# Performance work log

Hardware: AMD Instinct MI355X
Metric: run time of the kernel (lower is better)

## Reference

```python
import jax, jax.numpy as jnp
import numpy as np

NUM_COEFF = 32   # num_coeff_per_dim
NUM_POINTS = 64  # Chebyshev collocation points
MAX_ITERS = 10
TOL = 0.01
BATCH, DIM, HID, T_EVAL_N = 512, 256, 512, 16


def T_grid(t, n):
    # Chebyshev T_k(t), k=0..n-1 -> [n, len(t)]
    rows = [jnp.ones_like(t), t]
    for _ in range(2, n):
        rows.append(2.0 * t * rows[-1] - rows[-2])
    return jnp.stack(rows[:n])


def U_grid(t, n):
    rows = [jnp.ones_like(t), 2.0 * t]
    for _ in range(2, n):
        rows.append(2.0 * t * rows[-1] - rows[-2])
    return jnp.stack(rows[:n])


def DT_grid(t, n):
    # d/dt T_k = k * U_{k-1}
    return jnp.vstack([jnp.zeros((1, t.shape[0]), t.dtype),
                       U_grid(t, n - 1) * jnp.arange(1, n, dtype=t.dtype)[:, None]])


def vf_point(t, y, W1, b1, W2, b2):
    # f(t, y) for y [B, D], scalar t
    h = jnp.tanh(y @ W1 + b1 + t)
    return h @ W2 + b2


def vf_grid(t, y, W1, b1, W2, b2):
    # vectorized over Chebyshev points: y [B, D, P], t [P]
    h = jnp.tanh(jnp.einsum('bdp,dh->bhp', y, W1) + b1[None, :, None] + t[None, None, :])
    return jnp.einsum('bhp,hd->bdp', h, W2) + b2[None, :, None]


def setup_inputs() -> dict:
    key = jax.random.key(0)
    ks = jax.random.split(key, 7)
    s1 = 1.0 / np.sqrt(DIM)
    s2 = 1.0 / np.sqrt(HID)
    return {
        'y_init': jax.random.normal(ks[0], (BATCH, DIM), jnp.float32),
        't_eval': jnp.linspace(0.0, 1.0, T_EVAL_N, dtype=jnp.float32),
        'B_init': jax.random.uniform(ks[1], (BATCH, DIM, NUM_COEFF - 2), jnp.float32),
        'W1': jax.random.normal(ks[2], (DIM, HID), jnp.float32) * s1,
        'b1': jax.random.normal(ks[3], (HID,), jnp.float32) * 0.1,
        'W2': jax.random.normal(ks[4], (HID, DIM), jnp.float32) * s2,
        'b2': jax.random.normal(ks[5], (DIM,), jnp.float32) * 0.1,
    }


def _pan_solve(y_init, t_eval, B_init, W1, b1, W2, b2):
    t0, t1 = t_eval[0], t_eval[-1]
    dt = t_eval.dtype
    # time-independent spectral operators
    t_cheb = -jnp.sign(t1 - t0) * jnp.cos(jnp.pi * jnp.arange(NUM_POINTS, dtype=dt) / NUM_POINTS)
    Dt = jnp.diff(jnp.concatenate([t_cheb, jnp.ones((1,), dt)]))
    Phi = T_grid(t_cheb, NUM_COEFF)                        # [N, P]
    DPhi = (2.0 / (t1 - t0)) * DT_grid(t_cheb, NUM_COEFF)  # [N, P]
    inv0 = jnp.linalg.inv(jnp.stack([Phi[0:2, 0], DPhi[0:2, 0]]).T)  # [2,2]
    PD2 = jnp.stack([Phi[2:, 0], DPhi[2:, 0]], axis=-1)    # [N-2, 2]
    D01 = jnp.stack([DPhi[0, :], DPhi[1, :]], axis=0)      # [2, P]
    Phi_b = DPhi[2:, :] - PD2 @ inv0 @ D01                 # [N-2, P]
    Q = jnp.linalg.inv(Phi_b @ (Dt[:, None] * Phi_b.T))    # [N-2, N-2]
    PhibTQ = (Dt[:, None] * Phi_b.T) @ Q                   # [P, N-2]
    M2 = inv0 @ D01 @ PhibTQ                               # [2, N-2]

    f_init = vf_point(t0, y_init, W1, b1, W2, b2)
    yf2 = jnp.stack([y_init, f_init], axis=-1)             # [B, D, 2]

    def head(B_tail):
        return (yf2 - B_tail @ PD2) @ inv0                 # [B, D, 2]

    B = B_init
    done = jnp.array(False)
    delta = jnp.array(jnp.inf, dt)
    iters = jnp.array(0, jnp.int32)
    for _ in range(MAX_ITERS):  # Picard fixed-point iteration (masked early stop)
        B_prev = B
        B_full = jnp.concatenate([head(B_prev), B_prev], axis=-1)  # [B, D, N]
        y_grid = jnp.einsum('bdn,np->bdp', B_full, Phi)            # [B, D, P]
        fapprox = vf_grid(t_cheb, y_grid, W1, b1, W2, b2)          # [B, D, P]
        B_new = jnp.einsum('bdp,pn->bdn', fapprox, PhibTQ) - yf2 @ M2
        d = jnp.linalg.norm(B_new - B_prev)
        B = jnp.where(done, B_prev, B_new)
        delta = jnp.where(done, delta, d)
        iters = jnp.where(done, iters, iters + 1)
        done = done | (d < TOL)

    B_full = jnp.concatenate([head(B), B], axis=-1)
    t_out = -1.0 + 2.0 * (t_eval - t0) / (t1 - t0)
    Phi_out = T_grid(t_out, NUM_COEFF)                     # [N, T]
    traj = jnp.einsum('bdn,nt->tbd', B_full, Phi_out)      # [T, B, D]
    return traj, B, delta, iters


def reference(y_init, t_eval, B_init, W1, b1, W2, b2):
    traj, B, delta, iters = _pan_solve(y_init, t_eval, B_init, W1, b1, W2, b2)
    return (t_eval, traj, delta, B)
```

## Files before the change

### kernel.cpp

```cpp
#include <hip/hip_runtime.h>
#include <math.h>

#define NBATCH 512
#define NDIM 256
#define NHID 512
#define NC 32
#define NTAIL 30
#define NP 64
#define TEV 16
#define MAXIT 10
#define TOLF 0.01f
#define PI_F 3.14159265358979323846f

typedef __bf16 bf16_t;
typedef __bf16 bf16x8 __attribute__((ext_vector_type(8)));
typedef float f32x4 __attribute__((ext_vector_type(4)));
typedef unsigned short ushort_t;

constexpr size_t OFF_TCHEB = 0;
constexpr size_t OFF_PHIT  = 64;
constexpr size_t OFF_PD2I  = 2112;
constexpr size_t OFF_M2    = 2176;
constexpr size_t OFF_INV0  = 2240;
constexpr size_t OFF_PHIOUT= 2256;
constexpr size_t OFF_PQ    = 2768;
constexpr size_t OFF_PQBH  = 4816;
constexpr size_t OFF_PQBL  = 5840;
constexpr size_t OFF_PHIH  = 6864;
constexpr size_t OFF_PHIL  = 7888;
constexpr size_t OFF_SCAL  = 8912;
constexpr size_t OFF_H1F   = 8928;
constexpr size_t OFF_YF2I  = OFF_H1F + 262144;
constexpr size_t OFF_YFR   = OFF_YF2I + 262144;
constexpr size_t OFF_BT    = OFF_YFR + 3932160;
constexpr size_t OFF_W1T   = OFF_BT + 3932160;
constexpr size_t OFF_W2T   = OFF_W1T + 65536;
constexpr size_t WS_FLOATS = OFF_W2T + 65536;

constexpr size_t OUT_TEVAL = 0;
constexpr size_t OUT_TRAJ  = 16;
constexpr size_t OUT_DELTA = 16 + (size_t)TEV*NBATCH*NDIM;
constexpr size_t OUT_B     = OUT_DELTA + 1;

__device__ __forceinline__ ushort_t bf16bits(float v) {
    bf16_t h = (bf16_t)v; ushort_t u; __builtin_memcpy(&u, &h, 2); return u;
}
__device__ __forceinline__ float bf16val(ushort_t u) {
    bf16_t h; __builtin_memcpy(&h, &u, 2); return (float)h;
}

__global__ __launch_bounds__(512) void prologue_kernel(
    const float* __restrict__ t_eval, const float* __restrict__ y,
    const float* __restrict__ Bin,
    const float* __restrict__ W1, const float* __restrict__ b1,
    const float* __restrict__ W2, const float* __restrict__ b2,
    float* __restrict__ ws, float* __restrict__ out)
{
    struct SetupSh {
        double Gaug[30][61];
        double rowk[60];
        double colk[30];
        float Phi[32][64];
        float DPhi[32][64];
        float Phib[30][64];
        float tcs[64];
        float DtS[64];
        float inv0s[4];
        float pd2s[30][2];
    };
    __shared__ __align__(16) char pm[40960];
    static_assert(sizeof(SetupSh) <= 40960, "SetupSh too big");

    const int tid = threadIdx.x;
    const int role = blockIdx.x;

    if (role == 0) {
        SetupSh& S = *(SetupSh*)pm;
        const float t0 = t_eval[0], t1 = t_eval[TEV-1];
        const float sgn = (t1 > t0) ? 1.f : -1.f;

        if (tid < 64) {
            const float t = -sgn * cosf(PI_F * (float)tid / 64.f);
            S.tcs[tid] = t;
            float p0 = 1.f, p1 = t;
            S.Phi[0][tid] = p0; S.Phi[1][tid] = p1;
            for (int k = 2; k < 32; ++k) { float pk = 2.f*t*p1 - p0; S.Phi[k][tid] = pk; p0 = p1; p1 = pk; }
            const float sc = 2.f / (t1 - t0);
            float u0 = 1.f, u1 = 2.f*t;
            S.DPhi[0][tid] = 0.f;
            S.DPhi[1][tid] = sc * 1.f * u0;
            S.DPhi[2][tid] = sc * 2.f * u1;
            for (int k = 3; k < 32; ++k) { float uk = 2.f*t*u1 - u0; S.DPhi[k][tid] = sc * (float)k * uk; u0 = u1; u1 = uk; }
        }
        __syncthreads();
        if (tid < 64) S.DtS[tid] = ((tid < 63) ? S.tcs[tid+1] : 1.0f) - S.tcs[tid];
        if (tid == 0) {
            double a = S.Phi[0][0], b = S.DPhi[0][0], c = S.Phi[1][0], d = S.DPhi[1][0];
            double det = a*d - b*c;
            S.inv0s[0] = (float)( d/det); S.inv0s[1] = (float)(-b/det);
            S.inv0s[2] = (float)(-c/det); S.inv0s[3] = (float)( a/det);
        }
        __syncthreads();
        if (tid < 30) {
            float P = S.Phi[2+tid][0], D = S.DPhi[2+tid][0];
            float a0 = P*S.inv0s[0] + D*S.inv0s[2];
            float a1 = P*S.inv0s[1] + D*S.inv0s[3];
            S.pd2s[tid][0] = a0; S.pd2s[tid][1] = a1;
            ws[OFF_PD2I + tid*2+0] = a0;
            ws[OFF_PD2I + tid*2+1] = a1;
        }
        __syncthreads();
        if (tid < 64)
            for (int m = 0; m < 30; ++m)
                S.Phib[m][tid] = S.DPhi[2+m][tid] - (S.pd2s[m][0]*S.DPhi[0][tid] + S.pd2s[m][1]*S.DPhi[1][tid]);
        __syncthreads();

        for (int e = tid; e < 900; e += 512) {
            int i = e / 30, j = e % 30;
            double s = 0.0;
            for (int p = 0; p < 64; ++p) s += (double)S.Phib[i][p] * (double)S.DtS[p] * (double)S.Phib[j][p];
            S.Gaug[i][j] = s;
            S.Gaug[i][30+j] = (i == j) ? 1.0 : 0.0;
        }
        __syncthreads();

        for (int k = 0; k < 30; ++k) {
            double invpv = 1.0 / S.Gaug[k][k];
            if (tid < 60) S.rowk[tid] = S.Gaug[k][tid] * invpv;
            if (tid >= 64 && tid < 94) S.colk[tid-64] = S.Gaug[tid-64][k];
            __syncthreads();
            for (int e = tid; e < 1800; e += 512) {
                int i = e / 60, j = e - i*60;
                if (i == k) S.Gaug[i][j] = S.rowk[j];
                else        S.Gaug[i][j] -= S.colk[i] * S.rowk[j];
            }
            __syncthreads();
        }

        if (tid < 64) {
            ushort_t* pqh = (ushort_t*)(ws + OFF_PQBH);
            ushort_t* pql = (ushort_t*)(ws + OFF_PQBL);
            float pqrow[32];
            for (int n = 0; n < 30; ++n) {
                double s = 0.0;
                for (int m = 0; m < 30; ++m) s += (double)S.Phib[m][tid] * S.Gaug[m][30+n];
                pqrow[n] = (float)((double)S.DtS[tid] * s);
            }
            pqrow[30] = 0.f; pqrow[31] = 0.f;
            for (int n = 0; n < 32; ++n) {
                ws[OFF_PQ + (size_t)tid*32 + n] = pqrow[n];
                bf16_t h = (bf16_t)pqrow[n];
                float hf = (float)h;
                pqh[n*64 + tid] = bf16bits(pqrow[n]);
                pql[n*64 + tid] = bf16bits(pqrow[n] - hf);
            }
        }
        __syncthreads();

        if (tid < 30) {
            double a20 = 0.0, a21 = 0.0;
            for (int p = 0; p < 64; ++p) {
                double pq = (double)ws[OFF_PQ + (size_t)p*32 + tid];
                a20 += (double)S.DPhi[0][p] * pq;
                a21 += (double)S.DPhi[1][p] * pq;
            }
            ws[OFF_M2 + 0*32 + tid] = (float)((double)S.inv0s[0]*a20 + (double)S.inv0s[1]*a21);
            ws[OFF_M2 + 1*32 + tid] = (float)((double)S.inv0s[2]*a20 + (double)S.inv0s[3]*a21);
        }

        if (tid < 64) {
            ushort_t* phh = (ushort_t*)(ws + OFF_PHIH);
            ushort_t* phl = (ushort_t*)(ws + OFF_PHIL);
            for (int n = 0; n < 32; ++n) {
                float f = S.Phi[n][tid];
                ws[OFF_PHIT + (size_t)tid*32 + n] = f;
                ushort_t hb = bf16bits(f);
                phh[tid*32 + n] = hb;
                phl[tid*32 + n] = bf16bits(f - bf16val(hb));
            }
            ws[OFF_TCHEB + tid] = S.tcs[tid];
        }

        if (tid < TEV) {
            float te = t_eval[tid];
            out[OUT_TEVAL + tid] = te;
            float tt = -1.f + 2.f*(te - t0)/(t1 - t0);
            float q0 = 1.f, q1 = tt;
            ws[OFF_PHIOUT + (size_t)tid*32 + 0] = q0;
            ws[OFF_PHIOUT + (size_t)tid*32 + 1] = q1;
            for (int k = 2; k < 32; ++k) { float qk = 2.f*tt*q1 - q0; ws[OFF_PHIOUT + (size_t)tid*32 + k] = qk; q0 = q1; q1 = qk; }
        }

        if (tid == 0) {
            double* acc = (double*)(ws + OFF_SCAL);
            acc[0] = 0.0;
            int* ip = (int*)(ws + OFF_SCAL + 2);
            ip[0] = 0;
            ip[1] = 0;
        }
    } else if (role <= 128) {
        const int b0 = (role - 1) * 4;
        float* ys = (float*)pm;
        float* hs = (float*)pm + 1024;
        for (int e = tid; e < 1024; e += 512) {
            int bb = e >> 8, d = e & 255;
            ys[bb*256 + d] = y[(size_t)(b0+bb)*NDIM + d];
        }
        __syncthreads();
        {
            const float base = b1[tid] + t_eval[0];
            float a0 = base, a1 = base, a2 = base, a3 = base;
            for (int d = 0; d < NDIM; ++d) {
                float wv = W1[(size_t)d*NHID + tid];
                a0 += ys[0*256+d]*wv; a1 += ys[1*256+d]*wv;
                a2 += ys[2*256+d]*wv; a3 += ys[3*256+d]*wv;
            }
            hs[0*512+tid] = tanhf(a0); hs[1*512+tid] = tanhf(a1);
            hs[2*512+tid] = tanhf(a2); hs[3*512+tid] = tanhf(a3);
        }
        __syncthreads();
        if (tid < NDIM) {
            const float fb = b2[tid];
            float f0 = fb, f1 = fb, f2 = fb, f3 = fb;
            for (int h = 0; h < NHID; ++h) {
                float wv = W2[(size_t)h*NDIM + tid];
                f0 += hs[0*512+h]*wv; f1 += hs[1*512+h]*wv;
                f2 += hs[2*512+h]*wv; f3 += hs[3*512+h]*wv;
            }
            const float t0 = t_eval[0], t1 = t_eval[TEV-1];
            const float sgn = (t1 > t0) ? 1.f : -1.f;
            const float sc = 2.f / (t1 - t0);
            double a = 1.0, bb = 0.0, c = (double)(-sgn), d = (double)sc;
            double det = a*d - bb*c;
            const float i0 = (float)( d/det), i1 = (float)(-bb/det);
            const float i2 = (float)(-c/det), i3 = (float)( a/det);
            float* yf2i = ws + OFF_YF2I;
            float* yfr  = ws + OFF_YFR;
            float fv[4] = {f0, f1, f2, f3};
            #pragma unroll
            for (int bb2 = 0; bb2 < 4; ++bb2) {
                const int b = b0 + bb2;
                const float yv = ys[bb2*256 + tid];
                const float f = fv[bb2];
                yf2i[((size_t)b*2 + 0)*NDIM + tid] = yv*i0 + f*i2;
                yf2i[((size_t)b*2 + 1)*NDIM + tid] = yv*i1 + f*i3;
                yfr [((size_t)b*2 + 0)*NDIM + tid] = yv;
                yfr [((size_t)b*2 + 1)*NDIM + tid] = f;
            }
        }
    } else if (role <= 128 + NBATCH) {
        if (tid < NDIM) {
            const int b = role - 129;
            float* Bt = ws + OFF_BT;
            const float* src = Bin + ((size_t)(b*NDIM + tid)) * NTAIL;
            #pragma unroll
            for (int n = 0; n < NTAIL; ++n)
                Bt[((size_t)b*NTAIL + n)*NDIM + tid] = src[n];
        }
    } else {
        const bool isW1 = (role <= 128 + NBATCH + 32);
        const int idx = isW1 ? (role - 129 - NBATCH) : (role - 129 - NBATCH - 32);
        const int R = isW1 ? NDIM : NHID;
        const int C = isW1 ? NHID : NDIM;
        const float* W = isW1 ? W1 : W2;
        bf16_t* Wt = (bf16_t*)(ws + (isW1 ? OFF_W1T : OFF_W2T));
        const int nbx = R / 64;
        const int r0 = (idx % nbx) * 64, c0 = (idx / nbx) * 64;
        float (*Ls)[65] = (float(*)[65])pm;
        const int lr = tid >> 6, lc = tid & 63;
        #pragma unroll
        for (int i = 0; i < 8; ++i) {
            int rr = i*8 + lr;
            Ls[rr][lc] = W[(size_t)(r0+rr)*C + c0+lc];
        }
        __syncthreads();
        #pragma unroll
        for (int i = 0; i < 8; ++i) {
            int cc = i*8 + lr;
            Wt[(size_t)(c0+cc)*R + r0 + lc] = (bf16_t)Ls[lc][cc];
        }
    }
}

__global__ __launch_bounds__(512, 4) void iter_kernel(
    const float* __restrict__ pd2i, const float* __restrict__ yf2i, const float* __restrict__ tch,
    const bf16_t* __restrict__ W1t, const bf16_t* __restrict__ W2t,
    const float* __restrict__ b1f, const float* __restrict__ b2f,
    const ushort_t* __restrict__ PQhi, const ushort_t* __restrict__ PQlo,
    const ushort_t* __restrict__ phiH, const ushort_t* __restrict__ phiL,
    const float* __restrict__ yfr, const float* __restrict__ M2f,
    float* __restrict__ Bt,
    double* __restrict__ accum, int* __restrict__ counter,
    int* __restrict__ done, float* __restrict__ outDelta)
{
    if (*done) return;
    __shared__ float pd2s[32][2];
    __shared__ float tchS[64];
    __shared__ float m2S[64];
    __shared__ double redd[8];
    __shared__ __align__(16) char smemA[33792];
    __shared__ __align__(16) char smemB[17408];
    __shared__ __align__(16) ushort_t PQHs[32*72];
    __shared__ __align__(16) ushort_t PQLs[32*72];

    const int t = threadIdx.x;
    const int b = blockIdx.x;
    const int lane = t & 63, w = t >> 6;
    const int fr = lane & 15, quad = lane >> 4;

    if (t < 60) ((float*)pd2s)[t] = pd2i[t];
    if (t >= 64 && t < 128) tchS[t-64] = tch[t-64];
    if (t >= 128 && t < 192) m2S[t-128] = M2f[t-128];
    __syncthreads();

    if (t < 256) {
        float cf[32];
        #pragma unroll
        for (int n = 0; n < NTAIL; ++n) cf[2+n] = Bt[((size_t)b*NTAIL + n)*NDIM + t];
        float c0 = yf2i[((size_t)b*2 + 0)*NDIM + t];
        float c1 = yf2i[((size_t)b*2 + 1)*NDIM + t];
        #pragma unroll
        for (int n = 0; n < NTAIL; ++n) { c0 -= cf[2+n]*pd2s[n][0]; c1 -= cf[2+n]*pd2s[n][1]; }
        cf[0] = c0; cf[1] = c1;
        unsigned* BH32 = (unsigned*)smemA;
        unsigned* BL32 = (unsigned*)(smemA + 16384);
        #pragma unroll
        for (int n2 = 0; n2 < 16; ++n2) {
            float f0 = cf[2*n2], f1 = cf[2*n2+1];
            ushort_t h0 = bf16bits(f0), h1 = bf16bits(f1);
            ushort_t l0 = bf16bits(f0 - bf16val(h0)), l1 = bf16bits(f1 - bf16val(h1));
            int idx = t*16 + ((n2 >> 2) ^ (t & 3))*4 + (n2 & 3);
            BH32[idx] = (unsigned)h0 | ((unsigned)h1 << 16);
            BL32[idx] = (unsigned)l0 | ((unsigned)l1 << 16);
        }
    } else {
        int e = (t - 256) * 8;
        int r = e >> 6, c = e & 63;
        uint4 vh = *(const uint4*)(PQhi + e);
        uint4 vl = *(const uint4*)(PQlo + e);
        *(uint4*)(PQHs + r*72 + c) = vh;
        *(uint4*)(PQLs + r*72 + c) = vl;
    }
    __syncthreads();

    ushort_t* Ay = (ushort_t*)smemA;
    {
        bf16x8 bH[2], bL[2];
        const ushort_t* BHu = (const ushort_t*)smemA;
        const ushort_t* BLu = (const ushort_t*)(smemA + 16384);
        #pragma unroll
        for (int j = 0; j < 2; ++j) {
            const int d = w*32 + j*16 + fr;
            const int off = d*32 + (quad ^ (d & 3))*8;
            bH[j] = *(const bf16x8*)(BHu + off);
            bL[j] = *(const bf16x8*)(BLu + off);
        }
        bf16x8 aH[4], aL[4];
        #pragma unroll
        for (int i = 0; i < 4; ++i) {
            aH[i] = *(const bf16x8*)(phiH + (i*16 + fr)*32 + quad*8);
            aL[i] = *(const bf16x8*)(phiL + (i*16 + fr)*32 + quad*8);
        }
        __syncthreads();
        f32x4 accY[4][2];
        #pragma unroll
        for (int i = 0; i < 4; ++i)
            #pragma unroll
            for (int j = 0; j < 2; ++j) {
                f32x4 a = (f32x4){0.f,0.f,0.f,0.f};
                a = __builtin_amdgcn_mfma_f32_16x16x32_bf16(aH[i], bH[j], a, 0, 0, 0);
                a = __builtin_amdgcn_mfma_f32_16x16x32_bf16(aH[i], bL[j], a, 0, 0, 0);
                a = __builtin_amdgcn_mfma_f32_16x16x32_bf16(aL[i], bH[j], a, 0, 0, 0);
                accY[i][j] = a;
            }
        #pragma unroll
        for (int i = 0; i < 4; ++i)
            #pragma unroll
            for (int j = 0; j < 2; ++j)
                #pragma unroll
                for (int r = 0; r < 4; ++r) {
                    const int p = i*16 + quad*4 + r;
                    const int d = w*32 + j*16 + fr;
                    Ay[p*264 + d] = bf16bits(accY[i][j][r]);
                }
    }
    __syncthreads();

    ushort_t* Hc = (ushort_t*)smemB;
    f32x4 accF[4][2];
    #pragma unroll
    for (int i = 0; i < 4; ++i)
        #pragma unroll
        for (int j = 0; j < 2; ++j) accF[i][j] = (f32x4){0.f,0.f,0.f,0.f};

    #pragma unroll
    for (int pass = 0; pass < 4; ++pass) {
        bf16x8 w2f[4][2];
        #pragma unroll
        for (int kt4 = 0; kt4 < 4; ++kt4)
            #pragma unroll
            for (int j = 0; j < 2; ++j) {
                const int d = w*32 + j*16 + fr;
                w2f[kt4][j] = *(const bf16x8*)(W2t + (size_t)d*NHID + pass*128 + kt4*32 + quad*8);
            }
        f32x4 acc1[4];
        #pragma unroll
        for (int i = 0; i < 4; ++i) acc1[i] = (f32x4){0.f,0.f,0.f,0.f};
        #pragma unroll
        for (int kt = 0; kt < NDIM; kt += 32) {
            bf16x8 af[4], bfv;
            #pragma unroll
            for (int i = 0; i < 4; ++i)
                af[i] = *(const bf16x8*)(Ay + (i*16 + fr)*264 + kt + quad*8);
            {
                const int ncol = pass*128 + w*16 + fr;
                bfv = *(const bf16x8*)(W1t + (size_t)ncol*NDIM + kt + quad*8);
            }
            #pragma unroll
            for (int i = 0; i < 4; ++i)
                acc1[i] = __builtin_amdgcn_mfma_f32_16x16x32_bf16(af[i], bfv, acc1[i], 0, 0, 0);
        }
        __syncthreads();
        {
            const int col = w*16 + fr;
            const float bv = b1f[pass*128 + col];
            #pragma unroll
            for (int i = 0; i < 4; ++i)
                #pragma unroll
                for (int r = 0; r < 4; ++r) {
                    const int row = i*16 + quad*4 + r;
                    float v = acc1[i][r] + bv + tchS[row];
                    v = fminf(fmaxf(v, -15.f), 15.f);
                    float e = __expf(2.f*v);
                    Hc[row*136 + col] = bf16bits((e - 1.f)/(e + 1.f));
                }
        }
        __syncthreads();
        #pragma unroll
        for (int kt4 = 0; kt4 < 4; ++kt4) {
            bf16x8 af[4];
            #pragma unroll
            for (int i = 0; i < 4; ++i)
                af[i] = *(const bf16x8*)(Hc + (i*16 + fr)*136 + kt4*32 + quad*8);
            #pragma unroll
            for (int i = 0; i < 4; ++i)
                #pragma unroll
                for (int j = 0; j < 2; ++j)
                    accF[i][j] = __builtin_amdgcn_mfma_f32_16x16x32_bf16(af[i], w2f[kt4][j], accF[i][j], 0, 0, 0);
        }
    }
    __syncthreads();

    {
        unsigned* FsT32 = (unsigned*)smemA;
        #pragma unroll
        for (int i = 0; i < 4; ++i)
            #pragma unroll
            for (int j = 0; j < 2; ++j) {
                const int d = w*32 + j*16 + fr;
                const float bv = b2f[d];
                #pragma unroll
                for (int rp = 0; rp < 2; ++rp) {
                    unsigned u0 = bf16bits(accF[i][j][rp*2]   + bv);
                    unsigned u1 = bf16bits(accF[i][j][rp*2+1] + bv);
                    FsT32[d*33 + i*8 + quad*2 + rp] = u0 | (u1 << 16);
                }
            }
    }
    __syncthreads();

    double ss = 0.0;
    {
        const ushort_t* FsTu = (const ushort_t*)smemA;
        float yvv[2], ffv[2];
        #pragma unroll
        for (int j2 = 0; j2 < 2; ++j2) {
            const int d2 = w*32 + j2*16 + fr;
            yvv[j2] = yfr[((size_t)b*2 + 0)*NDIM + d2];
            ffv[j2] = yfr[((size_t)b*2 + 1)*NDIM + d2];
        }
        f32x4 acc2[2][2];
        #pragma unroll
        for (int m2 = 0; m2 < 2; ++m2)
            #pragma unroll
            for (int j2 = 0; j2 < 2; ++j2) acc2[m2][j2] = (f32x4){0.f,0.f,0.f,0.f};
        #pragma unroll
        for (int kk = 0; kk < 2; ++kk) {
            bf16x8 ah[2], al[2];
            #pragma unroll
            for (int m2 = 0; m2 < 2; ++m2) {
                const int off = (m2*16 + fr)*72 + kk*32 + quad*8;
                ah[m2] = *(const bf16x8*)(PQHs + off);
                al[m2] = *(const bf16x8*)(PQLs + off);
            }
            #pragma unroll
            for (int j2 = 0; j2 < 2; ++j2) {
                const int d2 = w*32 + j2*16 + fr;
                bf16x8 bfv = *(const bf16x8*)(FsTu + d2*66 + kk*32 + quad*8);
                #pragma unroll
                for (int m2 = 0; m2 < 2; ++m2) {
                    acc2[m2][j2] = __builtin_amdgcn_mfma_f32_16x16x32_bf16(ah[m2], bfv, acc2[m2][j2], 0, 0, 0);
                    acc2[m2][j2] = __builtin_amdgcn_mfma_f32_16x16x32_bf16(al[m2], bfv, acc2[m2][j2], 0, 0, 0);
                }
            }
        }
        #pragma unroll
        for (int m2 = 0; m2 < 2; ++m2)
            #pragma unroll
            for (int j2 = 0; j2 < 2; ++j2)
                #pragma unroll
                for (int rr = 0; rr < 4; ++rr) {
                    const int n = m2*16 + quad*4 + rr;
                    if (n < NTAIL) {
                        const int d = w*32 + j2*16 + fr;
                        const size_t idx = ((size_t)b*NTAIL + n)*NDIM + d;
                        float ym2v = yvv[j2]*m2S[n] + ffv[j2]*m2S[32 + n];
                        float val = acc2[m2][j2][rr] - ym2v;
                        float old = Bt[idx];
                        float diff = val - old;
                        Bt[idx] = val;
                        ss += (double)diff*(double)diff;
                    }
                }
    }

    #pragma unroll
    for (int off = 32; off > 0; off >>= 1) ss += __shfl_down(ss, off, 64);
    if (lane == 0) redd[w] = ss;
    __syncthreads();
    if (t == 0) {
        double tot = redd[0] + redd[1] + redd[2] + redd[3]
                   + redd[4] + redd[5] + redd[6] + redd[7];
        atomicAdd(accum, tot);
        __threadfence();
        int old = atomicAdd(counter, 1);
        if (old == 511) {
            unsigned long long raw = atomicExch((unsigned long long*)accum, 0ull);
            double total; __builtin_memcpy(&total, &raw, 8);
            float dl = (float)sqrt(total);
            *outDelta = dl;
            *counter = 0;
            if (dl < TOLF) *done = 1;
        }
    }
}

__global__ __launch_bounds__(256) void kernelEpi(const float* __restrict__ PhiOut, const float* __restrict__ pd2i,
                                                 const float* __restrict__ yf2i, const float* __restrict__ Bt,
                                                 float* __restrict__ outTraj, float* __restrict__ outB)
{
    __shared__ float Po[16][32];
    const int t = threadIdx.x, b = blockIdx.x;
    for (int i = t; i < 512; i += 256) ((float*)Po)[i] = PhiOut[i];
    __syncthreads();
    float cf[32];
    #pragma unroll
    for (int n = 0; n < NTAIL; ++n) cf[2+n] = Bt[((size_t)b*NTAIL + n)*NDIM + t];
    float c0 = yf2i[((size_t)b*2 + 0)*NDIM + t];
    float c1 = yf2i[((size_t)b*2 + 1)*NDIM + t];
    #pragma unroll
    for (int n = 0; n < NTAIL; ++n) { c0 -= cf[2+n]*pd2i[n*2]; c1 -= cf[2+n]*pd2i[n*2+1]; }
    cf[0] = c0; cf[1] = c1;
    for (int tt = 0; tt < TEV; ++tt) {
        float s = 0.f;
        #pragma unroll
        for (int k = 0; k < 32; ++k) s += cf[k]*Po[tt][k];
        outTraj[((size_t)tt*NBATCH + b)*NDIM + t] = s;
    }
    float* ob = outB + ((size_t)(b*NDIM + t))*NTAIL;
    #pragma unroll
    for (int n = 0; n < NTAIL; ++n) ob[n] = cf[2+n];
}

extern "C" void kernel_launch(void* const* d_in, const int* in_sizes, int n_in,
                              void* d_out, int out_size, void* d_ws, size_t ws_size,
                              hipStream_t stream)
{
    const float* y_init = (const float*)d_in[0];
    const float* t_eval = (const float*)d_in[1];
    const float* B_init = (const float*)d_in[2];
    const float* W1     = (const float*)d_in[3];
    const float* b1     = (const float*)d_in[4];
    const float* W2     = (const float*)d_in[5];
    const float* b2     = (const float*)d_in[6];
    float* out = (float*)d_out;
    float* ws  = (float*)d_ws;
    if (ws_size < WS_FLOATS * sizeof(float)) return;

    float* tcheb = ws + OFF_TCHEB;
    float* pd2i  = ws + OFF_PD2I;
    float* M2    = ws + OFF_M2;
    float* PhiOut= ws + OFF_PHIOUT;
    double* accum = (double*)(ws + OFF_SCAL);
    int* done    = (int*)(ws + OFF_SCAL + 2);
    int* counter = (int*)(ws + OFF_SCAL + 3);
    float* yf2i = ws + OFF_YF2I;
    float* yfr  = ws + OFF_YFR;
    float* Bt   = ws + OFF_BT;
    bf16_t* W1t = (bf16_t*)(ws + OFF_W1T);
    bf16_t* W2t = (bf16_t*)(ws + OFF_W2T);
    ushort_t* pqh = (ushort_t*)(ws + OFF_PQBH);
    ushort_t* pql = (ushort_t*)(ws + OFF_PQBL);
    ushort_t* phh = (ushort_t*)(ws + OFF_PHIH);
    ushort_t* phl = (ushort_t*)(ws + OFF_PHIL);

    prologue_kernel<<<1 + 128 + NBATCH + 64, 512, 0, stream>>>(
        t_eval, y_init, B_init, W1, b1, W2, b2, ws, out);

    for (int it = 0; it < MAXIT; ++it) {
        iter_kernel<<<NBATCH, 512, 0, stream>>>(pd2i, yf2i, tcheb, W1t, W2t, b1, b2,
                                                pqh, pql, phh, phl, yfr, M2, Bt,
                                                accum, counter, done, out + OUT_DELTA);
    }
    kernelEpi<<<NBATCH, 256, 0, stream>>>(PhiOut, pd2i, yf2i, Bt, out + OUT_TRAJ, out + OUT_B);
}
```

Baseline: 654.4 us.

## Fuse epilogue into last iteration, single-wave Gauss-Jordan, wider prologue batch tiles

Three separate changes. The epilogue kernel is folded into the final iter_kernel launch, which computes the trajectory and final coefficients after its last Picard step and removes one launch. The 30x30 Gauss-Jordan inverse in the prologue now runs on a single wavefront with wave barriers in place of block-wide __syncthreads, so its 60 serial steps no longer pay for full-block synchronisation. The initial vector-field blocks each handle 8 batch rows instead of 4, halving their count while doubling per-thread accumulators.

```diff
diff --git a/kernel.cpp b/kernel.cpp
--- a/kernel.cpp
+++ b/kernel.cpp
@@ -124,18 +124,21 @@
         }
         __syncthreads();
 
-        for (int k = 0; k < 30; ++k) {
-            double invpv = 1.0 / S.Gaug[k][k];
-            if (tid < 60) S.rowk[tid] = S.Gaug[k][tid] * invpv;
-            if (tid >= 64 && tid < 94) S.colk[tid-64] = S.Gaug[tid-64][k];
-            __syncthreads();
-            for (int e = tid; e < 1800; e += 512) {
-                int i = e / 60, j = e - i*60;
-                if (i == k) S.Gaug[i][j] = S.rowk[j];
-                else        S.Gaug[i][j] -= S.colk[i] * S.rowk[j];
-            }
-            __syncthreads();
-        }
+        if (tid < 64) {
+            for (int k = 0; k < 30; ++k) {
+                double invpv = 1.0 / S.Gaug[k][k];
+                if (tid < 60) S.rowk[tid] = S.Gaug[k][tid] * invpv;
+                if (tid < 30) S.colk[tid] = S.Gaug[tid][k];
+                __builtin_amdgcn_wave_barrier();
+                for (int e = tid; e < 1800; e += 64) {
+                    int i = e / 60, j = e - i*60;
+                    if (i == k) S.Gaug[i][j] = S.rowk[j];
+                    else        S.Gaug[i][j] -= S.colk[i] * S.rowk[j];
+                }
+                __builtin_amdgcn_wave_barrier();
+            }
+        }
+        __syncthreads();
 
         if (tid < 64) {
             ushort_t* pqh = (ushort_t*)(ws + OFF_PQBH);
@@ -198,34 +201,38 @@
             ip[0] = 0;
             ip[1] = 0;
         }
-    } else if (role <= 128) {
-        const int b0 = (role - 1) * 4;
+    } else if (role <= 64) {
+        const int b0 = (role - 1) * 8;
         float* ys = (float*)pm;
-        float* hs = (float*)pm + 1024;
-        for (int e = tid; e < 1024; e += 512) {
+        float* hs = (float*)pm + 2048;
+        for (int e = tid; e < 2048; e += 512) {
             int bb = e >> 8, d = e & 255;
             ys[bb*256 + d] = y[(size_t)(b0+bb)*NDIM + d];
         }
         __syncthreads();
         {
             const float base = b1[tid] + t_eval[0];
-            float a0 = base, a1 = base, a2 = base, a3 = base;
+            float a[8];
+            #pragma unroll
+            for (int i = 0; i < 8; ++i) a[i] = base;
             for (int d = 0; d < NDIM; ++d) {
                 float wv = W1[(size_t)d*NHID + tid];
-                a0 += ys[0*256+d]*wv; a1 += ys[1*256+d]*wv;
-                a2 += ys[2*256+d]*wv; a3 += ys[3*256+d]*wv;
-            }
-            hs[0*512+tid] = tanhf(a0); hs[1*512+tid] = tanhf(a1);
-            hs[2*512+tid] = tanhf(a2); hs[3*512+tid] = tanhf(a3);
+                #pragma unroll
+                for (int i = 0; i < 8; ++i) a[i] += ys[i*256 + d]*wv;
+            }
+            #pragma unroll
+            for (int i = 0; i < 8; ++i) hs[i*512 + tid] = tanhf(a[i]);
         }
         __syncthreads();
         if (tid < NDIM) {
             const float fb = b2[tid];
-            float f0 = fb, f1 = fb, f2 = fb, f3 = fb;
+            float f[8];
+            #pragma unroll
+            for (int i = 0; i < 8; ++i) f[i] = fb;
             for (int h = 0; h < NHID; ++h) {
                 float wv = W2[(size_t)h*NDIM + tid];
-                f0 += hs[0*512+h]*wv; f1 += hs[1*512+h]*wv;
-                f2 += hs[2*512+h]*wv; f3 += hs[3*512+h]*wv;
+                #pragma unroll
+                for (int i = 0; i < 8; ++i) f[i] += hs[i*512 + h]*wv;
             }
             const float t0 = t_eval[0], t1 = t_eval[TEV-1];
             const float sgn = (t1 > t0) ? 1.f : -1.f;
@@ -236,21 +243,20 @@
             const float i2 = (float)(-c/det), i3 = (float)( a/det);
             float* yf2i = ws + OFF_YF2I;
             float* yfr  = ws + OFF_YFR;
-            float fv[4] = {f0, f1, f2, f3};
-            #pragma unroll
-            for (int bb2 = 0; bb2 < 4; ++bb2) {
+            #pragma unroll
+            for (int bb2 = 0; bb2 < 8; ++bb2) {
                 const int b = b0 + bb2;
                 const float yv = ys[bb2*256 + tid];
-                const float f = fv[bb2];
-                yf2i[((size_t)b*2 + 0)*NDIM + tid] = yv*i0 + f*i2;
-                yf2i[((size_t)b*2 + 1)*NDIM + tid] = yv*i1 + f*i3;
+                const float fv = f[bb2];
+                yf2i[((size_t)b*2 + 0)*NDIM + tid] = yv*i0 + fv*i2;
+                yf2i[((size_t)b*2 + 1)*NDIM + tid] = yv*i1 + fv*i3;
                 yfr [((size_t)b*2 + 0)*NDIM + tid] = yv;
-                yfr [((size_t)b*2 + 1)*NDIM + tid] = f;
-            }
-        }
-    } else if (role <= 128 + NBATCH) {
+                yfr [((size_t)b*2 + 1)*NDIM + tid] = fv;
+            }
+        }
+    } else if (role <= 64 + NBATCH) {
         if (tid < NDIM) {
-            const int b = role - 129;
+            const int b = role - 65;
             float* Bt = ws + OFF_BT;
             const float* src = Bin + ((size_t)(b*NDIM + tid)) * NTAIL;
             #pragma unroll
@@ -258,8 +264,8 @@
                 Bt[((size_t)b*NTAIL + n)*NDIM + tid] = src[n];
         }
     } else {
-        const bool isW1 = (role <= 128 + NBATCH + 32);
-        const int idx = isW1 ? (role - 129 - NBATCH) : (role - 129 - NBATCH - 32);
+        const bool isW1 = (role <= 64 + NBATCH + 32);
+        const int idx = isW1 ? (role - 65 - NBATCH) : (role - 65 - NBATCH - 32);
         const int R = isW1 ? NDIM : NHID;
         const int C = isW1 ? NHID : NDIM;
         const float* W = isW1 ? W1 : W2;
@@ -291,9 +297,14 @@
     const float* __restrict__ yfr, const float* __restrict__ M2f,
     float* __restrict__ Bt,
     double* __restrict__ accum, int* __restrict__ counter,
-    int* __restrict__ done, float* __restrict__ outDelta)
+    int* __restrict__ done, float* __restrict__ outDelta,
+    const float* __restrict__ PhiOut, float* __restrict__ outTraj, float* __restrict__ outB,
+    int last)
 {
-    if (*done) return;
+    const bool runIter = (*done == 0);
+    const bool isLast = (last != 0);
+    if (!runIter && !isLast) return;
+
     __shared__ float pd2s[32][2];
     __shared__ float tchS[64];
     __shared__ float m2S[64];
@@ -313,263 +324,267 @@
     if (t >= 128 && t < 192) m2S[t-128] = M2f[t-128];
     __syncthreads();
 
-    if (t < 256) {
-        float cf[32];
-        #pragma unroll
-        for (int n = 0; n < NTAIL; ++n) cf[2+n] = Bt[((size_t)b*NTAIL + n)*NDIM + t];
-        float c0 = yf2i[((size_t)b*2 + 0)*NDIM + t];
-        float c1 = yf2i[((size_t)b*2 + 1)*NDIM + t];
-        #pragma unroll
-        for (int n = 0; n < NTAIL; ++n) { c0 -= cf[2+n]*pd2s[n][0]; c1 -= cf[2+n]*pd2s[n][1]; }
-        cf[0] = c0; cf[1] = c1;
-        unsigned* BH32 = (unsigned*)smemA;
-        unsigned* BL32 = (unsigned*)(smemA + 16384);
-        #pragma unroll
-        for (int n2 = 0; n2 < 16; ++n2) {
-            float f0 = cf[2*n2], f1 = cf[2*n2+1];
-            ushort_t h0 = bf16bits(f0), h1 = bf16bits(f1);
-            ushort_t l0 = bf16bits(f0 - bf16val(h0)), l1 = bf16bits(f1 - bf16val(h1));
-            int idx = t*16 + ((n2 >> 2) ^ (t & 3))*4 + (n2 & 3);
-            BH32[idx] = (unsigned)h0 | ((unsigned)h1 << 16);
-            BL32[idx] = (unsigned)l0 | ((unsigned)l1 << 16);
-        }
-    } else {
-        int e = (t - 256) * 8;
-        int r = e >> 6, c = e & 63;
-        uint4 vh = *(const uint4*)(PQhi + e);
-        uint4 vl = *(const uint4*)(PQlo + e);
-        *(uint4*)(PQHs + r*72 + c) = vh;
-        *(uint4*)(PQLs + r*72 + c) = vl;
-    }
-    __syncthreads();
-
-    ushort_t* Ay = (ushort_t*)smemA;
-    {
-        bf16x8 bH[2], bL[2];
-        const ushort_t* BHu = (const ushort_t*)smemA;
-        const ushort_t* BLu = (const ushort_t*)(smemA + 16384);
-        #pragma unroll
-        for (int j = 0; j < 2; ++j) {
-            const int d = w*32 + j*16 + fr;
-            const int off = d*32 + (quad ^ (d & 3))*8;
-            bH[j] = *(const bf16x8*)(BHu + off);
-            bL[j] = *(const bf16x8*)(BLu + off);
-        }
-        bf16x8 aH[4], aL[4];
-        #pragma unroll
-        for (int i = 0; i < 4; ++i) {
-            aH[i] = *(const bf16x8*)(phiH + (i*16 + fr)*32 + quad*8);
-            aL[i] = *(const bf16x8*)(phiL + (i*16 + fr)*32 + quad*8);
-        }
-        __syncthreads();
-        f32x4 accY[4][2];
+    if (runIter) {
+        if (t < 256) {
+            float cf[32];
+            #pragma unroll
+            for (int n = 0; n < NTAIL; ++n) cf[2+n] = Bt[((size_t)b*NTAIL + n)*NDIM + t];
+            float c0 = yf2i[((size_t)b*2 + 0)*NDIM + t];
+            float c1 = yf2i[((size_t)b*2 + 1)*NDIM + t];
+            #pragma unroll
+            for (int n = 0; n < NTAIL; ++n) { c0 -= cf[2+n]*pd2s[n][0]; c1 -= cf[2+n]*pd2s[n][1]; }
+            cf[0] = c0; cf[1] = c1;
+            unsigned* BH32 = (unsigned*)smemA;
+            unsigned* BL32 = (unsigned*)(smemA + 16384);
+            #pragma unroll
+            for (int n2 = 0; n2 < 16; ++n2) {
+                float f0 = cf[2*n2], f1 = cf[2*n2+1];
+                ushort_t h0 = bf16bits(f0), h1 = bf16bits(f1);
+                ushort_t l0 = bf16bits(f0 - bf16val(h0)), l1 = bf16bits(f1 - bf16val(h1));
+                int idx = t*16 + ((n2 >> 2) ^ (t & 3))*4 + (n2 & 3);
+                BH32[idx] = (unsigned)h0 | ((unsigned)h1 << 16);
+                BL32[idx] = (unsigned)l0 | ((unsigned)l1 << 16);
+            }
+        } else {
+            int e = (t - 256) * 8;
+            int r = e >> 6, c = e & 63;
+            uint4 vh = *(const uint4*)(PQhi + e);
+            uint4 vl = *(const uint4*)(PQlo + e);
+            *(uint4*)(PQHs + r*72 + c) = vh;
+            *(uint4*)(PQLs + r*72 + c) = vl;
+        }
+        __syncthreads();
+
+        ushort_t* Ay = (ushort_t*)smemA;
+        {
+            bf16x8 bH[2], bL[2];
+            const ushort_t* BHu = (const ushort_t*)smemA;
+            const ushort_t* BLu = (const ushort_t*)(smemA + 16384);
+            #pragma unroll
+            for (int j = 0; j < 2; ++j) {
+                const int d = w*32 + j*16 + fr;
+                const int off = d*32 + (quad ^ (d & 3))*8;
+                bH[j] = *(const bf16x8*)(BHu + off);
+                bL[j] = *(const bf16x8*)(BLu + off);
+            }
+            bf16x8 aH[4], aL[4];
+            #pragma unroll
+            for (int i = 0; i < 4; ++i) {
+                aH[i] = *(const bf16x8*)(phiH + (i*16 + fr)*32 + quad*8);
+                aL[i] = *(const bf16x8*)(phiL + (i*16 + fr)*32 + quad*8);
+            }
+            __syncthreads();
+            f32x4 accY[4][2];
+            #pragma unroll
+            for (int i = 0; i < 4; ++i)
+                #pragma unroll
+                for (int j = 0; j < 2; ++j) {
+                    f32x4 a = (f32x4){0.f,0.f,0.f,0.f};
+                    a = __builtin_amdgcn_mfma_f32_16x16x32_bf16(aH[i], bH[j], a, 0, 0, 0);
+                    a = __builtin_amdgcn_mfma_f32_16x16x32_bf16(aH[i], bL[j], a, 0, 0, 0);
+                    a = __builtin_amdgcn_mfma_f32_16x16x32_bf16(aL[i], bH[j], a, 0, 0, 0);
+                    accY[i][j] = a;
+                }
+            #pragma unroll
+            for (int i = 0; i < 4; ++i)
+                #pragma unroll
+                for (int j = 0; j < 2; ++j)
+                    #pragma unroll
+                    for (int r = 0; r < 4; ++r) {
+                        const int p = i*16 + quad*4 + r;
+                        const int d = w*32 + j*16 + fr;
+                        Ay[p*264 + d] = bf16bits(accY[i][j][r]);
+                    }
+        }
+        __syncthreads();
+
+        ushort_t* Hc = (ushort_t*)smemB;
+        f32x4 accF[4][2];
         #pragma unroll
         for (int i = 0; i < 4; ++i)
             #pragma unroll
-            for (int j = 0; j < 2; ++j) {
-                f32x4 a = (f32x4){0.f,0.f,0.f,0.f};
-                a = __builtin_amdgcn_mfma_f32_16x16x32_bf16(aH[i], bH[j], a, 0, 0, 0);
-                a = __builtin_amdgcn_mfma_f32_16x16x32_bf16(aH[i], bL[j], a, 0, 0, 0);
-                a = __builtin_amdgcn_mfma_f32_16x16x32_bf16(aL[i], bH[j], a, 0, 0, 0);
-                accY[i][j] = a;
-            }
+            for (int j = 0; j < 2; ++j) accF[i][j] = (f32x4){0.f,0.f,0.f,0.f};
+
         #pragma unroll
-        for (int i = 0; i < 4; ++i)
-            #pragma unroll
-            for (int j = 0; j < 2; ++j)
-                #pragma unroll
-                for (int r = 0; r < 4; ++r) {
-                    const int p = i*16 + quad*4 + r;
+        for (int pass = 0; pass < 4; ++pass) {
+            bf16x8 w2f[4][2];
+            #pragma unroll
+            for (int kt4 = 0; kt4 < 4; ++kt4)
+                #pragma unroll
+                for (int j = 0; j < 2; ++j) {
                     const int d = w*32 + j*16 + fr;
-                    Ay[p*264 + d] = bf16bits(accY[i][j][r]);
+                    w2f[kt4][j] = *(const bf16x8*)(W2t + (size_t)d*NHID + pass*128 + kt4*32 + quad*8);
                 }
-    }
-    __syncthreads();
-
-    ushort_t* Hc = (ushort_t*)smemB;
-    f32x4 accF[4][2];
-    #pragma unroll
-    for (int i = 0; i < 4; ++i)
-        #pragma unroll
-        for (int j = 0; j < 2; ++j) accF[i][j] = (f32x4){0.f,0.f,0.f,0.f};
-
-    #pragma unroll
-    for (int pass = 0; pass < 4; ++pass) {
-        bf16x8 w2f[4][2];
-        #pragma unroll
-        for (int kt4 = 0; kt4 < 4; ++kt4)
-            #pragma unroll
-            for (int j = 0; j < 2; ++j) {
-                const int d = w*32 + j*16 + fr;
-                w2f[kt4][j] = *(const bf16x8*)(W2t + (size_t)d*NHID + pass*128 + kt4*32 + quad*8);
-            }
-        f32x4 acc1[4];
-        #pragma unroll
-        for (int i = 0; i < 4; ++i) acc1[i] = (f32x4){0.f,0.f,0.f,0.f};
-        #pragma unroll
-        for (int kt = 0; kt < NDIM; kt += 32) {
-            bf16x8 af[4], bfv;
+            f32x4 acc1[4];
+            #pragma unroll
+            for (int i = 0; i < 4; ++i) acc1[i] = (f32x4){0.f,0.f,0.f,0.f};
+            #pragma unroll
+            for (int kt = 0; kt < NDIM; kt += 32) {
+                bf16x8 af[4], bfv;
+                #pragma unroll
+                for (int i = 0; i < 4; ++i)
+                    af[i] = *(const bf16x8*)(Ay + (i*16 + fr)*264 + kt + quad*8);
+                {
+                    const int ncol = pass*128 + w*16 + fr;
+                    bfv = *(const bf16x8*)(W1t + (size_t)ncol*NDIM + kt + quad*8);
+                }
+                #pragma unroll
+                for (int i = 0; i < 4; ++i)
+                    acc1[i] = __builtin_amdgcn_mfma_f32_16x16x32_bf16(af[i], bfv, acc1[i], 0, 0, 0);
+            }
+            __syncthreads();
+            {
+                const int col = w*16 + fr;
+                const float bv = b1f[pass*128 + col];
+                #pragma unroll
+                for (int i = 0; i < 4; ++i)
+                    #pragma unroll
+                    for (int r = 0; r < 4; ++r) {
+                        const int row = i*16 + quad*4 + r;
+                        float v = acc1[i][r] + bv + tchS[row];
+                        v = fminf(fmaxf(v, -15.f), 15.f);
+                        float e = __expf(2.f*v);
+                        Hc[row*136 + col] = bf16bits((e - 1.f)/(e + 1.f));
+                    }
+            }
+            __syncthreads();
+            #pragma unroll
+            for (int kt4 = 0; kt4 < 4; ++kt4) {
+                bf16x8 af[4];
+                #pragma unroll
+                for (int i = 0; i < 4; ++i)
+                    af[i] = *(const bf16x8*)(Hc + (i*16 + fr)*136 + kt4*32 + quad*8);
+                #pragma unroll
+                for (int i = 0; i < 4; ++i)
+                    #pragma unroll
+                    for (int j = 0; j < 2; ++j)
+                        accF[i][j] = __builtin_amdgcn_mfma_f32_16x16x32_bf16(af[i], w2f[kt4][j], accF[i][j], 0, 0, 0);
+            }
+        }
+        __syncthreads();
+
+        {
+            unsigned* FsT32 = (unsigned*)smemA;
             #pragma unroll
             for (int i = 0; i < 4; ++i)
-                af[i] = *(const bf16x8*)(Ay + (i*16 + fr)*264 + kt + quad*8);
-            {
-                const int ncol = pass*128 + w*16 + fr;
-                bfv = *(const bf16x8*)(W1t + (size_t)ncol*NDIM + kt + quad*8);
-            }
-            #pragma unroll
-            for (int i = 0; i < 4; ++i)
-                acc1[i] = __builtin_amdgcn_mfma_f32_16x16x32_bf16(af[i], bfv, acc1[i], 0, 0, 0);
-        }
-        __syncthreads();
+                #pragma unroll
+                for (int j = 0; j < 2; ++j) {
+                    const int d = w*32 + j*16 + fr;
+                    const float bv = b2f[d];
+                    #pragma unroll
+                    for (int rp = 0; rp < 2; ++rp) {
+                        unsigned u0 = bf16bits(accF[i][j][rp*2]   + bv);
+                        unsigned u1 = bf16bits(accF[i][j][rp*2+1] + bv);
+                        FsT32[d*33 + i*8 + quad*2 + rp] = u0 | (u1 << 16);
+                    }
+                }
+        }
+        __syncthreads();
+
+        double ss = 0.0;
         {
-            const int col = w*16 + fr;
-            const float bv = b1f[pass*128 + col];
-            #pragma unroll
-            for (int i = 0; i < 4; ++i)
-                #pragma unroll
-                for (int r = 0; r < 4; ++r) {
-                    const int row = i*16 + quad*4 + r;
-                    float v = acc1[i][r] + bv + tchS[row];
-                    v = fminf(fmaxf(v, -15.f), 15.f);
-                    float e = __expf(2.f*v);
-                    Hc[row*136 + col] = bf16bits((e - 1.f)/(e + 1.f));
-                }
-        }
-        __syncthreads();
-        #pragma unroll
-        for (int kt4 = 0; kt4 < 4; ++kt4) {
-            bf16x8 af[4];
-            #pragma unroll
-            for (int i = 0; i < 4; ++i)
-                af[i] = *(const bf16x8*)(Hc + (i*16 + fr)*136 + kt4*32 + quad*8);
-            #pragma unroll
-            for (int i = 0; i < 4; ++i)
-                #pragma unroll
-                for (int j = 0; j < 2; ++j)
-                    accF[i][j] = __builtin_amdgcn_mfma_f32_16x16x32_bf16(af[i], w2f[kt4][j], accF[i][j], 0, 0, 0);
-        }
-    }
-    __syncthreads();
-
-    {
-        unsigned* FsT32 = (unsigned*)smemA;
-        #pragma unroll
-        for (int i = 0; i < 4; ++i)
-            #pragma unroll
-            for (int j = 0; j < 2; ++j) {
-                const int d = w*32 + j*16 + fr;
-                const float bv = b2f[d];
-                #pragma unroll
-                for (int rp = 0; rp < 2; ++rp) {
-                    unsigned u0 = bf16bits(accF[i][j][rp*2]   + bv);
-                    unsigned u1 = bf16bits(accF[i][j][rp*2+1] + bv);
-                    FsT32[d*33 + i*8 + quad*2 + rp] = u0 | (u1 << 16);
-                }
-            }
-    }
-    __syncthreads();
-
-    double ss = 0.0;
-    {
-        const ushort_t* FsTu = (const ushort_t*)smemA;
-        float yvv[2], ffv[2];
-        #pragma unroll
-        for (int j2 = 0; j2 < 2; ++j2) {
-            const int d2 = w*32 + j2*16 + fr;
-            yvv[j2] = yfr[((size_t)b*2 + 0)*NDIM + d2];
-            ffv[j2] = yfr[((size_t)b*2 + 1)*NDIM + d2];
-        }
-        f32x4 acc2[2][2];
-        #pragma unroll
-        for (int m2 = 0; m2 < 2; ++m2)
-            #pragma unroll
-            for (int j2 = 0; j2 < 2; ++j2) acc2[m2][j2] = (f32x4){0.f,0.f,0.f,0.f};
-        #pragma unroll
-        for (int kk = 0; kk < 2; ++kk) {
-            bf16x8 ah[2], al[2];
-            #pragma unroll
-            for (int m2 = 0; m2 < 2; ++m2) {
-                const int off = (m2*16 + fr)*72 + kk*32 + quad*8;
-                ah[m2] = *(const bf16x8*)(PQHs + off);
-                al[m2] = *(const bf16x8*)(PQLs + off);
-            }
+            const ushort_t* FsTu = (const ushort_t*)smemA;
+            float yvv[2], ffv[2];
             #pragma unroll
             for (int j2 = 0; j2 < 2; ++j2) {
                 const int d2 = w*32 + j2*16 + fr;
-                bf16x8 bfv = *(const bf16x8*)(FsTu + d2*66 + kk*32 + quad*8);
+                yvv[j2] = yfr[((size_t)b*2 + 0)*NDIM + d2];
+                ffv[j2] = yfr[((size_t)b*2 + 1)*NDIM + d2];
+            }
+            f32x4 acc2[2][2];
+            #pragma unroll
+            for (int m2 = 0; m2 < 2; ++m2)
+                #pragma unroll
+                for (int j2 = 0; j2 < 2; ++j2) acc2[m2][j2] = (f32x4){0.f,0.f,0.f,0.f};
+            #pragma unroll
+            for (int kk = 0; kk < 2; ++kk) {
+                bf16x8 ah[2], al[2];
                 #pragma unroll
                 for (int m2 = 0; m2 < 2; ++m2) {
-                    acc2[m2][j2] = __builtin_amdgcn_mfma_f32_16x16x32_bf16(ah[m2], bfv, acc2[m2][j2], 0, 0, 0);
-                    acc2[m2][j2] = __builtin_amdgcn_mfma_f32_16x16x32_bf16(al[m2], bfv, acc2[m2][j2], 0, 0, 0);
+                    const int off = (m2*16 + fr)*72 + kk*32 + quad*8;
+                    ah[m2] = *(const bf16x8*)(PQHs + off);
+                    al[m2] = *(const bf16x8*)(PQLs + off);
                 }
-            }
-        }
-        #pragma unroll
-        for (int m2 = 0; m2 < 2; ++m2)
-            #pragma unroll
-            for (int j2 = 0; j2 < 2; ++j2)
-                #pragma unroll
-                for (int rr = 0; rr < 4; ++rr) {
-                    const int n = m2*16 + quad*4 + rr;
-                    if (n < NTAIL) {
-                        const int d = w*32 + j2*16 + fr;
-                        const size_t idx = ((size_t)b*NTAIL + n)*NDIM + d;
-                        float ym2v = yvv[j2]*m2S[n] + ffv[j2]*m2S[32 + n];
-                        float val = acc2[m2][j2][rr] - ym2v;
-                        float old = Bt[idx];
-                        float diff = val - old;
-                        Bt[idx] = val;
-                        ss += (double)diff*(double)diff;
+                #pragma unroll
+                for (int j2 = 0; j2 < 2; ++j2) {
+                    const int d2 = w*32 + j2*16 + fr;
+                    bf16x8 bfv = *(const bf16x8*)(FsTu + d2*66 + kk*32 + quad*8);
+                    #pragma unroll
+                    for (int m2 = 0; m2 < 2; ++m2) {
+                        acc2[m2][j2] = __builtin_amdgcn_mfma_f32_16x16x32_bf16(ah[m2], bfv, acc2[m2][j2], 0, 0, 0);
+                        acc2[m2][j2] = __builtin_amdgcn_mfma_f32_16x16x32_bf16(al[m2], bfv, acc2[m2][j2], 0, 0, 0);
                     }
                 }
+            }
+            #pragma unroll
+            for (int m2 = 0; m2 < 2; ++m2)
+                #pragma unroll
+                for (int j2 = 0; j2 < 2; ++j2)
+                    #pragma unroll
+                    for (int rr = 0; rr < 4; ++rr) {
+                        const int n = m2*16 + quad*4 + rr;
+                        if (n < NTAIL) {
+                            const int d = w*32 + j2*16 + fr;
+                            const size_t idx = ((size_t)b*NTAIL + n)*NDIM + d;
+                            float ym2v = yvv[j2]*m2S[n] + ffv[j2]*m2S[32 + n];
+                            float val = acc2[m2][j2][rr] - ym2v;
+                            float old = Bt[idx];
+                            float diff = val - old;
+                            Bt[idx] = val;
+                            ss += (double)diff*(double)diff;
+                        }
+                    }
+        }
+
+        #pragma unroll
+        for (int off = 32; off > 0; off >>= 1) ss += __shfl_down(ss, off, 64);
+        if (lane == 0) redd[w] = ss;
+        __syncthreads();
+        if (t == 0) {
+            double tot = redd[0] + redd[1] + redd[2] + redd[3]
+                       + redd[4] + redd[5] + redd[6] + redd[7];
+            atomicAdd(accum, tot);
+            __threadfence();
+            int old = atomicAdd(counter, 1);
+            if (old == 511) {
+                unsigned long long raw = atomicExch((unsigned long long*)accum, 0ull);
+                double total; __builtin_memcpy(&total, &raw, 8);
+                float dl = (float)sqrt(total);
+                *outDelta = dl;
+                *counter = 0;
+                if (dl < TOLF) *done = 1;
+            }
+        }
     }
 
-    #pragma unroll
-    for (int off = 32; off > 0; off >>= 1) ss += __shfl_down(ss, off, 64);
-    if (lane == 0) redd[w] = ss;
-    __syncthreads();
-    if (t == 0) {
-        double tot = redd[0] + redd[1] + redd[2] + redd[3]
-                   + redd[4] + redd[5] + redd[6] + redd[7];
-        atomicAdd(accum, tot);
-        __threadfence();
-        int old = atomicAdd(counter, 1);
-        if (old == 511) {
-            unsigned long long raw = atomicExch((unsigned long long*)accum, 0ull);
-            double total; __builtin_memcpy(&total, &raw, 8);
-            float dl = (float)sqrt(total);
-            *outDelta = dl;
-            *counter = 0;
-            if (dl < TOLF) *done = 1;
+    if (isLast) {
+        __syncthreads();
+        {
+            float* Po = (float*)smemB;
+            if (t < 512) Po[t] = PhiOut[t];
+        }
+        __syncthreads();
+        if (t < 256) {
+            const float* Po = (const float*)smemB;
+            float cf[32];
+            #pragma unroll
+            for (int n = 0; n < NTAIL; ++n) cf[2+n] = Bt[((size_t)b*NTAIL + n)*NDIM + t];
+            float c0 = yf2i[((size_t)b*2 + 0)*NDIM + t];
+            float c1 = yf2i[((size_t)b*2 + 1)*NDIM + t];
+            #pragma unroll
+            for (int n = 0; n < NTAIL; ++n) { c0 -= cf[2+n]*pd2s[n][0]; c1 -= cf[2+n]*pd2s[n][1]; }
+            cf[0] = c0; cf[1] = c1;
+            for (int tt = 0; tt < TEV; ++tt) {
+                float s = 0.f;
+                #pragma unroll
+                for (int k = 0; k < 32; ++k) s += cf[k]*Po[tt*32 + k];
+                outTraj[((size_t)tt*NBATCH + b)*NDIM + t] = s;
+            }
+            float* ob = outB + ((size_t)(b*NDIM + t))*NTAIL;
+            #pragma unroll
+            for (int n = 0; n < NTAIL; ++n) ob[n] = cf[2+n];
         }
     }
-}
-
-__global__ __launch_bounds__(256) void kernelEpi(const float* __restrict__ PhiOut, const float* __restrict__ pd2i,
-                                                 const float* __restrict__ yf2i, const float* __restrict__ Bt,
-                                                 float* __restrict__ outTraj, float* __restrict__ outB)
-{
-    __shared__ float Po[16][32];
-    const int t = threadIdx.x, b = blockIdx.x;
-    for (int i = t; i < 512; i += 256) ((float*)Po)[i] = PhiOut[i];
-    __syncthreads();
-    float cf[32];
-    #pragma unroll
-    for (int n = 0; n < NTAIL; ++n) cf[2+n] = Bt[((size_t)b*NTAIL + n)*NDIM + t];
-    float c0 = yf2i[((size_t)b*2 + 0)*NDIM + t];
-    float c1 = yf2i[((size_t)b*2 + 1)*NDIM + t];
-    #pragma unroll
-    for (int n = 0; n < NTAIL; ++n) { c0 -= cf[2+n]*pd2i[n*2]; c1 -= cf[2+n]*pd2i[n*2+1]; }
-    cf[0] = c0; cf[1] = c1;
-    for (int tt = 0; tt < TEV; ++tt) {
-        float s = 0.f;
-        #pragma unroll
-        for (int k = 0; k < 32; ++k) s += cf[k]*Po[tt][k];
-        outTraj[((size_t)tt*NBATCH + b)*NDIM + t] = s;
-    }
-    float* ob = outB + ((size_t)(b*NDIM + t))*NTAIL;
-    #pragma unroll
-    for (int n = 0; n < NTAIL; ++n) ob[n] = cf[2+n];
 }
 
 extern "C" void kernel_launch(void* const* d_in, const int* in_sizes, int n_in,
@@ -604,13 +619,14 @@
     ushort_t* phh = (ushort_t*)(ws + OFF_PHIH);
     ushort_t* phl = (ushort_t*)(ws + OFF_PHIL);
 
-    prologue_kernel<<<1 + 128 + NBATCH + 64, 512, 0, stream>>>(
+    prologue_kernel<<<1 + 64 + NBATCH + 64, 512, 0, stream>>>(
         t_eval, y_init, B_init, W1, b1, W2, b2, ws, out);
 
     for (int it = 0; it < MAXIT; ++it) {
         iter_kernel<<<NBATCH, 512, 0, stream>>>(pd2i, yf2i, tcheb, W1t, W2t, b1, b2,
                                                 pqh, pql, phh, phl, yfr, M2, Bt,
-                                                accum, counter, done, out + OUT_DELTA);
+                                                accum, counter, done, out + OUT_DELTA,
+                                                PhiOut, out + OUT_TRAJ, out + OUT_B,
+                                                (it == MAXIT-1) ? 1 : 0);
     }
-    kernelEpi<<<NBATCH, 256, 0, stream>>>(PhiOut, pd2i, yf2i, Bt, out + OUT_TRAJ, out + OUT_B);
 }
```

New measurement: 752.4 us. +15.0%, slower.
